# Optimization experiments

Hardware: AMD Instinct MI355X
Metric: run time of the kernel (lower is better)

## Reference

```python
import jax, jax.numpy as jnp
import numpy as np

B, S, H, E = 2, 2048, 16, 64
INV_SCALE = 8.0  # sqrt(head_dim); forward divides scores by this


def setup_inputs() -> dict:
    key = jax.random.key(0)
    ks = jax.random.split(key, 10)
    return {
        "query": jax.random.normal(ks[0], (B, S, H, E), dtype=jnp.float32),
        "key": jax.random.normal(ks[1], (B, S, H, E), dtype=jnp.float32),
        "value": jax.random.normal(ks[2], (B, S, H, E), dtype=jnp.float32),
        "attn_mask": jax.random.randint(ks[3], (B, S), 0, 2, dtype=jnp.int32),
        "Wq": jax.random.normal(ks[4], (E, E), dtype=jnp.float32) / np.sqrt(E),
        "bq": jax.random.normal(ks[5], (E,), dtype=jnp.float32) * 0.02,
        "Wk": jax.random.normal(ks[6], (E, E), dtype=jnp.float32) / np.sqrt(E),
        "bk": jax.random.normal(ks[7], (E,), dtype=jnp.float32) * 0.02,
        "Wv": jax.random.normal(ks[8], (E, E), dtype=jnp.float32) / np.sqrt(E),
        "bv": jax.random.normal(ks[9], (E,), dtype=jnp.float32) * 0.02,
    }


def reference(query, key, value, attn_mask, Wq, bq, Wk, bk, Wv, bv):
    # Linear projections over the last (embed) dim; torch Linear: x @ W.T + b
    q = jnp.einsum('bshe,fe->bhsf', query, Wq) + bq  # [B,H,S,E] (permute 0,2,1,3 fused)
    k = jnp.einsum('bshe,fe->bhsf', key, Wk) + bk
    v = jnp.einsum('bshe,fe->bhsf', value, Wv) + bv
    scores = jnp.einsum('bhqe,bhke->bhqk', q, k) / INV_SCALE  # [B,H,S,S]
    # mask: positions where attn_mask == 0 get -inf, broadcast over (1,1,k_len)
    masked = attn_mask[:, None, None, :] == 0  # [B,1,1,S]
    scores = jnp.where(masked, -jnp.inf, scores)
    attn = jax.nn.softmax(scores, axis=-1)
    out = jnp.einsum('bhqk,bhke->bqhe', attn, v)  # permute back to [B,S,H,E]
    return out
```

## Files before the change

kernel.cpp:

```cpp
#include <hip/hip_runtime.h>


#define BATCH 2
#define SEQ   2048
#define NH    16
#define DE    64
#define LDOF  68
#define NKT   (SEQ / 64)
#define LOG2E 1.44269504088896340736f
#define CSHIFT 16.0f

using bf16x8   = __attribute__((ext_vector_type(8))) __bf16;
using bf16x4   = __attribute__((ext_vector_type(4))) __bf16;
using bf16x2   = __attribute__((ext_vector_type(2))) __bf16;
using floatx2  = __attribute__((ext_vector_type(2))) float;
using floatx4  = __attribute__((ext_vector_type(4))) float;
using floatx16 = __attribute__((ext_vector_type(16))) float;
using ushortx4 = __attribute__((ext_vector_type(4))) unsigned short;
using ushortx8 = __attribute__((ext_vector_type(8))) unsigned short;
using uintx4   = __attribute__((ext_vector_type(4))) unsigned int;
using intx4    = __attribute__((ext_vector_type(4))) int;

__device__ __forceinline__ ushortx4 cvt4(floatx4 f) {
    bf16x4 h = __builtin_convertvector(f, bf16x4);
    return __builtin_bit_cast(ushortx4, h);
}

__device__ __forceinline__ unsigned int pkbf16(float a, float b) {
    floatx2 f = {a, b};
    return __builtin_bit_cast(unsigned int, __builtin_convertvector(f, bf16x2));
}

__device__ __forceinline__ void pl32swap(unsigned int& x, unsigned int& y) {
    __asm__ volatile("v_permlane32_swap_b32 %0, %1" : "+v"(x), "+v"(y));
}

__global__ __launch_bounds__(256) void proj_kernel(
    const float* __restrict__ xq, const float* __restrict__ xk, const float* __restrict__ xv,
    const float* __restrict__ Wq, const float* __restrict__ bq,
    const float* __restrict__ Wk, const float* __restrict__ bk,
    const float* __restrict__ Wv, const float* __restrict__ bv,
    unsigned short* __restrict__ qb, unsigned short* __restrict__ kb,
    unsigned short* __restrict__ vtb)
{
    __shared__ __align__(16) unsigned short Wb[64 * 72];
    __shared__ __align__(16) unsigned short Xb[8 * 1160];
    __shared__ __align__(16) unsigned short Ob[12288];
    __shared__ float blds[64];

    const int t  = threadIdx.x;
    const int bi = blockIdx.x;
    const int hh = bi & 1;
    const int st = (bi >> 1) & 127;
    const int b  = (bi >> 8) & 1;
    const int p  = bi >> 9;
    const int h0 = hh * 8;
    const int lane = t & 63, w = t >> 6, quad = lane >> 4, l16 = lane & 15;

    const float* x    = (p == 0) ? xq : (p == 1) ? xk : xv;
    const float* W    = (p == 0) ? Wq : (p == 1) ? Wk : Wv;
    const float* bias = (p == 0) ? bq : (p == 1) ? bk : bv;

    #pragma unroll
    for (int i = 0; i < 8; ++i) {
        int idx = i * 256 + t;
        int s = idx >> 7, rem = idx & 127, h = rem >> 4, e4 = (rem & 15) * 4;
        floatx4 xv4 = *(const floatx4*)(x + ((size_t)(b * SEQ + st * 16 + s) * NH + h0 + h) * DE + e4);
        *(ushortx4*)&Xb[h * 1160 + s * 72 + e4] = cvt4(xv4);
    }
    #pragma unroll
    for (int i = 0; i < 4; ++i) {
        int idx = i * 256 + t;
        int row = idx >> 4, c4 = (idx & 15) * 4;
        floatx4 wv4 = *(const floatx4*)(W + row * 64 + c4);
        *(ushortx4*)&Wb[row * 72 + c4] = cvt4(wv4);
    }
    if (t < 64) blds[t] = bias[t];
    __syncthreads();

    if (p < 2) {
        bf16x8 a0 = *(const bf16x8*)&Wb[(w * 16 + l16) * 72 + quad * 8];
        bf16x8 a1 = *(const bf16x8*)&Wb[(w * 16 + l16) * 72 + 32 + quad * 8];
        floatx4 bf4 = *(const floatx4*)&blds[w * 16 + quad * 4];
        const float scale = (p == 0) ? 0.125f * LOG2E : 1.0f;
        #pragma unroll
        for (int h = 0; h < 8; ++h) {
            bf16x8 b0 = *(const bf16x8*)&Xb[h * 1160 + l16 * 72 + quad * 8];
            bf16x8 b1 = *(const bf16x8*)&Xb[h * 1160 + l16 * 72 + 32 + quad * 8];
            floatx4 c = {0.f, 0.f, 0.f, 0.f};
            c = __builtin_amdgcn_mfma_f32_16x16x32_bf16(a0, b0, c, 0, 0, 0);
            c = __builtin_amdgcn_mfma_f32_16x16x32_bf16(a1, b1, c, 0, 0, 0);
            floatx4 v;
            v[0] = (c[0] + bf4[0]) * scale; v[1] = (c[1] + bf4[1]) * scale;
            v[2] = (c[2] + bf4[2]) * scale; v[3] = (c[3] + bf4[3]) * scale;
            *(ushortx4*)&Ob[h * 1160 + l16 * 72 + w * 16 + quad * 4] = cvt4(v);
        }
    } else {
        bf16x8 b0 = *(const bf16x8*)&Wb[(w * 16 + l16) * 72 + quad * 8];
        bf16x8 b1 = *(const bf16x8*)&Wb[(w * 16 + l16) * 72 + 32 + quad * 8];
        const float bw = blds[w * 16 + l16];
        #pragma unroll
        for (int h = 0; h < 8; ++h) {
            bf16x8 a0 = *(const bf16x8*)&Xb[h * 1160 + l16 * 72 + quad * 8];
            bf16x8 a1 = *(const bf16x8*)&Xb[h * 1160 + l16 * 72 + 32 + quad * 8];
            floatx4 c = {0.f, 0.f, 0.f, 0.f};
            c = __builtin_amdgcn_mfma_f32_16x16x32_bf16(a0, b0, c, 0, 0, 0);
            c = __builtin_amdgcn_mfma_f32_16x16x32_bf16(a1, b1, c, 0, 0, 0);
            floatx4 v;
            v[0] = c[0] + bw; v[1] = c[1] + bw; v[2] = c[2] + bw; v[3] = c[3] + bw;
            *(ushortx4*)&Ob[h * 1536 + (w * 16 + l16) * 24 + quad * 4] = cvt4(v);
        }
    }
    __syncthreads();

    if (p < 2) {
        unsigned short* dst = (p == 0) ? qb : kb;
        const int rb  = st >> 1;
        const int sl0 = (st & 1) * 16;
        #pragma unroll
        for (int i = 0; i < 4; ++i) {
            int idx = i * 256 + t;
            int j = idx & 7, s = (idx >> 3) & 15, h = idx >> 7;
            ushortx8 v = *(const ushortx8*)&Ob[h * 1160 + s * 72 + j * 8];
            size_t off = ((size_t)((b * 16 + h0 + h) * 64) + rb) * 2048 + j * 256 + (sl0 + s) * 8;
            *(ushortx8*)(dst + off) = v;
        }
    } else {
        const int kt  = st >> 2;
        const int cb  = (st & 3) * 2;
        #pragma unroll
        for (int i = 0; i < 4; ++i) {
            int idx = i * 256 + t;
            int cl = idx & 1, e = (idx >> 1) & 63, h = idx >> 7;
            ushortx8 v = *(const ushortx8*)&Ob[h * 1536 + e * 24 + cl * 8];
            size_t off = (((size_t)(b * 16 + h0 + h) * 32 + kt) * 8 + cb + cl) * 512 + e * 8;
            *(ushortx8*)(vtb + off) = v;
        }
    }
}

__global__ __launch_bounds__(512, 4) void attn_kernel(
    const unsigned short* __restrict__ qb, const unsigned short* __restrict__ kb,
    const unsigned short* __restrict__ vtb, const int* __restrict__ mask,
    float* __restrict__ out)
{
    __shared__ __align__(16) char smem[36864 + 8192];
    float* Ol = (float*)smem;
    float* Ll = (float*)(smem + 34816);
    float* Ml = (float*)(smem + 36864);

    const int wg  = blockIdx.x;
    const int bh  = ((wg >> 3) >> 4) * 8 + (wg & 7);
    const int qt  = (wg >> 3) & 15;
    const int b   = bh >> 4, h = bh & 15;
    const int q0  = qt * 128;
    const int t   = threadIdx.x;
    const int lane = t & 63, w = t >> 6;
    const int hi = lane >> 5, l31 = lane & 31;
    const int qw = w & 3, kblk = w >> 2;

    {
        intx4 mv = *(const intx4*)(mask + b * SEQ + t * 4);
        Ml[t * 4 + 0] = mv[0] ? -CSHIFT : -1e30f;
        Ml[t * 4 + 1] = mv[1] ? -CSHIFT : -1e30f;
        Ml[t * 4 + 2] = mv[2] ? -CSHIFT : -1e30f;
        Ml[t * 4 + 3] = mv[3] ? -CSHIFT : -1e30f;
    }

    const unsigned short* qp = qb + ((size_t)(bh * 64 + qt * 4 + qw)) * 2048 + hi * 256 + l31 * 8;
    bf16x8 qf[4];
    #pragma unroll
    for (int ks = 0; ks < 4; ++ks)
        qf[ks] = *(const bf16x8*)(qp + ks * 512);

    const unsigned short* kp = kb + ((size_t)(bh * 64 + kblk)) * 2048 + hi * 256 + l31 * 8;
    const unsigned short* vp = vtb + (size_t)bh * 131072 + (kblk * 4 + hi) * 512 + l31 * 8;
    const float* Mb = Ml + kblk * 32 + hi * 4;

    __syncthreads();

    floatx16 o0, o1;
    #pragma unroll
    for (int i = 0; i < 16; ++i) { o0[i] = 0.f; o1[i] = 0.f; }
    float lp = 0.f;

    for (int kt = 0; kt < NKT; ++kt) {
        const unsigned short* kq = kp + kt * 4096;
        bf16x8 kf0 = *(const bf16x8*)(kq);
        bf16x8 kf1 = *(const bf16x8*)(kq + 512);
        bf16x8 kf2 = *(const bf16x8*)(kq + 1024);
        bf16x8 kf3 = *(const bf16x8*)(kq + 1536);

        const float* Mc = Mb + kt * 64;
        floatx16 sc;
        #pragma unroll
        for (int g = 0; g < 4; ++g) {
            floatx4 mb = *(const floatx4*)(Mc + g * 8);
            sc[4 * g + 0] = mb[0]; sc[4 * g + 1] = mb[1];
            sc[4 * g + 2] = mb[2]; sc[4 * g + 3] = mb[3];
        }
        sc = __builtin_amdgcn_mfma_f32_32x32x16_bf16(kf0, qf[0], sc, 0, 0, 0);
        sc = __builtin_amdgcn_mfma_f32_32x32x16_bf16(kf1, qf[1], sc, 0, 0, 0);
        sc = __builtin_amdgcn_mfma_f32_32x32x16_bf16(kf2, qf[2], sc, 0, 0, 0);
        sc = __builtin_amdgcn_mfma_f32_32x32x16_bf16(kf3, qf[3], sc, 0, 0, 0);

        const unsigned short* vq = vp + kt * 4096;
        bf16x8 vf00 = *(const bf16x8*)(vq);
        bf16x8 vf01 = *(const bf16x8*)(vq + 256);
        bf16x8 vf10 = *(const bf16x8*)(vq + 1024);
        bf16x8 vf11 = *(const bf16x8*)(vq + 1280);

        #pragma unroll
        for (int r = 0; r < 16; ++r)
            sc[r] = __builtin_amdgcn_exp2f(sc[r]);
        {
            float a0 = sc[0] + sc[1],   a1 = sc[2] + sc[3];
            float a2 = sc[4] + sc[5],   a3 = sc[6] + sc[7];
            float a4 = sc[8] + sc[9],   a5 = sc[10] + sc[11];
            float a6 = sc[12] + sc[13], a7 = sc[14] + sc[15];
            lp += ((a0 + a1) + (a2 + a3)) + ((a4 + a5) + (a6 + a7));
        }

        unsigned int wd0 = pkbf16(sc[0], sc[1]),   wd1 = pkbf16(sc[2], sc[3]);
        unsigned int wd2 = pkbf16(sc[4], sc[5]),   wd3 = pkbf16(sc[6], sc[7]);
        unsigned int wd4 = pkbf16(sc[8], sc[9]),   wd5 = pkbf16(sc[10], sc[11]);
        unsigned int wd6 = pkbf16(sc[12], sc[13]), wd7 = pkbf16(sc[14], sc[15]);
        pl32swap(wd0, wd2); pl32swap(wd1, wd3);
        pl32swap(wd4, wd6); pl32swap(wd5, wd7);
        uintx4 f0v = {wd0, wd1, wd2, wd3};
        uintx4 f1v = {wd4, wd5, wd6, wd7};
        bf16x8 pf0 = __builtin_bit_cast(bf16x8, f0v);
        bf16x8 pf1 = __builtin_bit_cast(bf16x8, f1v);

        o0 = __builtin_amdgcn_mfma_f32_32x32x16_bf16(vf00, pf0, o0, 0, 0, 0);
        o1 = __builtin_amdgcn_mfma_f32_32x32x16_bf16(vf01, pf0, o1, 0, 0, 0);
        o0 = __builtin_amdgcn_mfma_f32_32x32x16_bf16(vf10, pf1, o0, 0, 0, 0);
        o1 = __builtin_amdgcn_mfma_f32_32x32x16_bf16(vf11, pf1, o1, 0, 0, 0);
    }

    const int qrow = qw * 32 + l31;
    Ll[qrow * 4 + kblk * 2 + hi] = lp;
    if (kblk == 1) {
        #pragma unroll
        for (int g = 0; g < 4; ++g) {
            floatx4 t0 = {o0[4*g+0], o0[4*g+1], o0[4*g+2], o0[4*g+3]};
            *(floatx4*)&Ol[qrow * LDOF + g * 8 + hi * 4] = t0;
            floatx4 t1 = {o1[4*g+0], o1[4*g+1], o1[4*g+2], o1[4*g+3]};
            *(floatx4*)&Ol[qrow * LDOF + 32 + g * 8 + hi * 4] = t1;
        }
    }
    __syncthreads();
    if (kblk == 0) {
        floatx4 lv = *(const floatx4*)&Ll[qrow * 4];
        float invl = __builtin_amdgcn_rcpf(lv[0] + lv[1] + lv[2] + lv[3]);
        #pragma unroll
        for (int g = 0; g < 4; ++g) {
            floatx4 t0 = *(floatx4*)&Ol[qrow * LDOF + g * 8 + hi * 4];
            t0[0] = (t0[0] + o0[4*g+0]) * invl; t0[1] = (t0[1] + o0[4*g+1]) * invl;
            t0[2] = (t0[2] + o0[4*g+2]) * invl; t0[3] = (t0[3] + o0[4*g+3]) * invl;
            *(floatx4*)&Ol[qrow * LDOF + g * 8 + hi * 4] = t0;
            floatx4 t1 = *(floatx4*)&Ol[qrow * LDOF + 32 + g * 8 + hi * 4];
            t1[0] = (t1[0] + o1[4*g+0]) * invl; t1[1] = (t1[1] + o1[4*g+1]) * invl;
            t1[2] = (t1[2] + o1[4*g+2]) * invl; t1[3] = (t1[3] + o1[4*g+3]) * invl;
            *(floatx4*)&Ol[qrow * LDOF + 32 + g * 8 + hi * 4] = t1;
        }
    }
    __syncthreads();
    {
        const int quad = lane >> 4, l16 = lane & 15;
        #pragma unroll
        for (int pass = 0; pass < 4; ++pass) {
            int rl  = w * 16 + pass * 4 + quad;
            int col = l16 * 4;
            floatx4 tv = *(const floatx4*)&Ol[rl * LDOF + col];
            *(floatx4*)(out + (((size_t)b * SEQ + q0 + rl) * NH + h) * DE + col) = tv;
        }
    }
}

extern "C" void kernel_launch(void* const* d_in, const int* in_sizes, int n_in,
                              void* d_out, int out_size, void* d_ws, size_t ws_size,
                              hipStream_t stream) {
    const float* query = (const float*)d_in[0];
    const float* key   = (const float*)d_in[1];
    const float* value = (const float*)d_in[2];
    const int*   mask  = (const int*)d_in[3];
    const float* Wq = (const float*)d_in[4];
    const float* bq = (const float*)d_in[5];
    const float* Wk = (const float*)d_in[6];
    const float* bk = (const float*)d_in[7];
    const float* Wv = (const float*)d_in[8];
    const float* bv = (const float*)d_in[9];

    const size_t tensor_elems = (size_t)BATCH * NH * SEQ * DE;
    unsigned short* qb  = (unsigned short*)d_ws;
    unsigned short* kb  = qb + tensor_elems;
    unsigned short* vtb = kb + tensor_elems;

    proj_kernel<<<dim3(3 * BATCH * 128 * 2), 256, 0, stream>>>(
        query, key, value, Wq, bq, Wk, bk, Wv, bv, qb, kb, vtb);
    attn_kernel<<<dim3(512), 512, 0, stream>>>(
        qb, kb, vtb, mask, (float*)d_out);
}
```

Baseline: 152.0 us.

## Split attention waves into two q-rows by four key-split groups with LDS-staged Q

Reorganises the 8 waves of each attention block so that each wave handles two 32-row query tiles (64 rows) against one quarter of the key tiles, instead of one query tile against half the keys. Each K and V fragment loaded from global memory is now reused for two query tiles, which halves K/V global traffic per block. Q is staged into LDS with global_load_lds and read from there, and s_setprio brackets the MFMA groups. The trade-offs are a four-way partial-output reduction in LDS with extra barriers, more accumulator registers (four 16-float accumulators), and LDS reads of Q on every iteration.

```diff
diff --git a/kernel.cpp b/kernel.cpp
--- a/kernel.cpp
+++ b/kernel.cpp
@@ -33,6 +33,12 @@
 
 __device__ __forceinline__ void pl32swap(unsigned int& x, unsigned int& y) {
     __asm__ volatile("v_permlane32_swap_b32 %0, %1" : "+v"(x), "+v"(y));
+}
+
+__device__ __forceinline__ void glds16(const unsigned short* g, unsigned short* l) {
+    __builtin_amdgcn_global_load_lds(
+        (const __attribute__((address_space(1))) unsigned int*)g,
+        (__attribute__((address_space(3))) unsigned int*)l, 16, 0, 0);
 }
 
 __global__ __launch_bounds__(256) void proj_kernel(
@@ -144,10 +150,11 @@
     const unsigned short* __restrict__ vtb, const int* __restrict__ mask,
     float* __restrict__ out)
 {
-    __shared__ __align__(16) char smem[36864 + 8192];
+    __shared__ __align__(16) char smem[38912];
+    unsigned short* Qlds = (unsigned short*)smem;
+    float* Ml = (float*)(smem + 16384);
     float* Ol = (float*)smem;
     float* Ll = (float*)(smem + 34816);
-    float* Ml = (float*)(smem + 36864);
 
     const int wg  = blockIdx.x;
     const int bh  = ((wg >> 3) >> 4) * 8 + (wg & 7);
@@ -157,8 +164,12 @@
     const int t   = threadIdx.x;
     const int lane = t & 63, w = t >> 6;
     const int hi = lane >> 5, l31 = lane & 31;
-    const int qw = w & 3, kblk = w >> 2;
-
+    const int qw = w & 1, kblk = (w >> 1) & 1, par = w >> 2;
+    const int rid = par * 2 + kblk;
+
+    const unsigned short* qsrc = qb + ((size_t)(bh * 64 + qt * 4)) * 2048;
+    glds16(qsrc + w * 512 + lane * 8,        Qlds + w * 512);
+    glds16(qsrc + 4096 + w * 512 + lane * 8, Qlds + 4096 + w * 512);
     {
         intx4 mv = *(const intx4*)(mask + b * SEQ + t * 4);
         Ml[t * 4 + 0] = mv[0] ? -CSHIFT : -1e30f;
@@ -166,103 +177,197 @@
         Ml[t * 4 + 2] = mv[2] ? -CSHIFT : -1e30f;
         Ml[t * 4 + 3] = mv[3] ? -CSHIFT : -1e30f;
     }
-
-    const unsigned short* qp = qb + ((size_t)(bh * 64 + qt * 4 + qw)) * 2048 + hi * 256 + l31 * 8;
-    bf16x8 qf[4];
+    __syncthreads();
+
+    const unsigned short* kp = kb + ((size_t)(bh * 64 + kblk)) * 2048
+                               + (size_t)par * 4096 + hi * 256 + l31 * 8;
+    const unsigned short* vp = vtb + (size_t)bh * 131072 + (size_t)par * 4096
+                               + (kblk * 4 + hi) * 512 + l31 * 8;
+    const float* Mlb = Ml + par * 64 + kblk * 32 + hi * 4;
+    const unsigned short* qba = Qlds + (qw * 2) * 2048 + hi * 256 + l31 * 8;
+
+    floatx16 oa0, oa1, ob0, ob1;
     #pragma unroll
-    for (int ks = 0; ks < 4; ++ks)
-        qf[ks] = *(const bf16x8*)(qp + ks * 512);
-
-    const unsigned short* kp = kb + ((size_t)(bh * 64 + kblk)) * 2048 + hi * 256 + l31 * 8;
-    const unsigned short* vp = vtb + (size_t)bh * 131072 + (kblk * 4 + hi) * 512 + l31 * 8;
-    const float* Mb = Ml + kblk * 32 + hi * 4;
-
-    __syncthreads();
-
-    floatx16 o0, o1;
-    #pragma unroll
-    for (int i = 0; i < 16; ++i) { o0[i] = 0.f; o1[i] = 0.f; }
-    float lp = 0.f;
-
-    for (int kt = 0; kt < NKT; ++kt) {
-        const unsigned short* kq = kp + kt * 4096;
+    for (int i = 0; i < 16; ++i) { oa0[i] = 0.f; oa1[i] = 0.f; ob0[i] = 0.f; ob1[i] = 0.f; }
+    float lpa = 0.f, lpb = 0.f;
+
+    for (int it = 0; it < NKT / 2; ++it) {
+        const unsigned short* kq = kp + (size_t)it * 8192;
         bf16x8 kf0 = *(const bf16x8*)(kq);
         bf16x8 kf1 = *(const bf16x8*)(kq + 512);
         bf16x8 kf2 = *(const bf16x8*)(kq + 1024);
         bf16x8 kf3 = *(const bf16x8*)(kq + 1536);
-
-        const float* Mc = Mb + kt * 64;
-        floatx16 sc;
-        #pragma unroll
-        for (int g = 0; g < 4; ++g) {
-            floatx4 mb = *(const floatx4*)(Mc + g * 8);
-            sc[4 * g + 0] = mb[0]; sc[4 * g + 1] = mb[1];
-            sc[4 * g + 2] = mb[2]; sc[4 * g + 3] = mb[3];
-        }
-        sc = __builtin_amdgcn_mfma_f32_32x32x16_bf16(kf0, qf[0], sc, 0, 0, 0);
-        sc = __builtin_amdgcn_mfma_f32_32x32x16_bf16(kf1, qf[1], sc, 0, 0, 0);
-        sc = __builtin_amdgcn_mfma_f32_32x32x16_bf16(kf2, qf[2], sc, 0, 0, 0);
-        sc = __builtin_amdgcn_mfma_f32_32x32x16_bf16(kf3, qf[3], sc, 0, 0, 0);
-
-        const unsigned short* vq = vp + kt * 4096;
+        const float* Mc = Mlb + it * 128;
+        floatx4 m0 = *(const floatx4*)(Mc);
+        floatx4 m1 = *(const floatx4*)(Mc + 8);
+        floatx4 m2 = *(const floatx4*)(Mc + 16);
+        floatx4 m3 = *(const floatx4*)(Mc + 24);
+
+        floatx16 sa;
+        #pragma unroll
+        for (int j = 0; j < 4; ++j) {
+            sa[j] = m0[j]; sa[4 + j] = m1[j]; sa[8 + j] = m2[j]; sa[12 + j] = m3[j];
+        }
+        __builtin_amdgcn_s_setprio(1);
+        sa = __builtin_amdgcn_mfma_f32_32x32x16_bf16(kf0, *(const bf16x8*)(qba), sa, 0, 0, 0);
+        sa = __builtin_amdgcn_mfma_f32_32x32x16_bf16(kf1, *(const bf16x8*)(qba + 512), sa, 0, 0, 0);
+        sa = __builtin_amdgcn_mfma_f32_32x32x16_bf16(kf2, *(const bf16x8*)(qba + 1024), sa, 0, 0, 0);
+        sa = __builtin_amdgcn_mfma_f32_32x32x16_bf16(kf3, *(const bf16x8*)(qba + 1536), sa, 0, 0, 0);
+        __builtin_amdgcn_s_setprio(0);
+        #pragma unroll
+        for (int r = 0; r < 16; ++r) sa[r] = __builtin_amdgcn_exp2f(sa[r]);
+        {
+            float a0 = sa[0] + sa[1],   a1 = sa[2] + sa[3];
+            float a2 = sa[4] + sa[5],   a3 = sa[6] + sa[7];
+            float a4 = sa[8] + sa[9],   a5 = sa[10] + sa[11];
+            float a6 = sa[12] + sa[13], a7 = sa[14] + sa[15];
+            lpa += ((a0 + a1) + (a2 + a3)) + ((a4 + a5) + (a6 + a7));
+        }
+        unsigned int aw0 = pkbf16(sa[0], sa[1]),   aw1 = pkbf16(sa[2], sa[3]);
+        unsigned int aw2 = pkbf16(sa[4], sa[5]),   aw3 = pkbf16(sa[6], sa[7]);
+        unsigned int aw4 = pkbf16(sa[8], sa[9]),   aw5 = pkbf16(sa[10], sa[11]);
+        unsigned int aw6 = pkbf16(sa[12], sa[13]), aw7 = pkbf16(sa[14], sa[15]);
+        pl32swap(aw0, aw2); pl32swap(aw1, aw3);
+        pl32swap(aw4, aw6); pl32swap(aw5, aw7);
+        uintx4 fa0 = {aw0, aw1, aw2, aw3};
+        uintx4 fa1 = {aw4, aw5, aw6, aw7};
+        bf16x8 pf0a = __builtin_bit_cast(bf16x8, fa0);
+        bf16x8 pf1a = __builtin_bit_cast(bf16x8, fa1);
+
+        floatx16 sb;
+        #pragma unroll
+        for (int j = 0; j < 4; ++j) {
+            sb[j] = m0[j]; sb[4 + j] = m1[j]; sb[8 + j] = m2[j]; sb[12 + j] = m3[j];
+        }
+        __builtin_amdgcn_s_setprio(1);
+        sb = __builtin_amdgcn_mfma_f32_32x32x16_bf16(kf0, *(const bf16x8*)(qba + 2048), sb, 0, 0, 0);
+        sb = __builtin_amdgcn_mfma_f32_32x32x16_bf16(kf1, *(const bf16x8*)(qba + 2560), sb, 0, 0, 0);
+        sb = __builtin_amdgcn_mfma_f32_32x32x16_bf16(kf2, *(const bf16x8*)(qba + 3072), sb, 0, 0, 0);
+        sb = __builtin_amdgcn_mfma_f32_32x32x16_bf16(kf3, *(const bf16x8*)(qba + 3584), sb, 0, 0, 0);
+        __builtin_amdgcn_s_setprio(0);
+
+        const unsigned short* vq = vp + (size_t)it * 8192;
         bf16x8 vf00 = *(const bf16x8*)(vq);
         bf16x8 vf01 = *(const bf16x8*)(vq + 256);
         bf16x8 vf10 = *(const bf16x8*)(vq + 1024);
         bf16x8 vf11 = *(const bf16x8*)(vq + 1280);
 
         #pragma unroll
-        for (int r = 0; r < 16; ++r)
-            sc[r] = __builtin_amdgcn_exp2f(sc[r]);
+        for (int r = 0; r < 16; ++r) sb[r] = __builtin_amdgcn_exp2f(sb[r]);
         {
-            float a0 = sc[0] + sc[1],   a1 = sc[2] + sc[3];
-            float a2 = sc[4] + sc[5],   a3 = sc[6] + sc[7];
-            float a4 = sc[8] + sc[9],   a5 = sc[10] + sc[11];
-            float a6 = sc[12] + sc[13], a7 = sc[14] + sc[15];
-            lp += ((a0 + a1) + (a2 + a3)) + ((a4 + a5) + (a6 + a7));
-        }
-
-        unsigned int wd0 = pkbf16(sc[0], sc[1]),   wd1 = pkbf16(sc[2], sc[3]);
-        unsigned int wd2 = pkbf16(sc[4], sc[5]),   wd3 = pkbf16(sc[6], sc[7]);
-        unsigned int wd4 = pkbf16(sc[8], sc[9]),   wd5 = pkbf16(sc[10], sc[11]);
-        unsigned int wd6 = pkbf16(sc[12], sc[13]), wd7 = pkbf16(sc[14], sc[15]);
-        pl32swap(wd0, wd2); pl32swap(wd1, wd3);
-        pl32swap(wd4, wd6); pl32swap(wd5, wd7);
-        uintx4 f0v = {wd0, wd1, wd2, wd3};
-        uintx4 f1v = {wd4, wd5, wd6, wd7};
-        bf16x8 pf0 = __builtin_bit_cast(bf16x8, f0v);
-        bf16x8 pf1 = __builtin_bit_cast(bf16x8, f1v);
-
-        o0 = __builtin_amdgcn_mfma_f32_32x32x16_bf16(vf00, pf0, o0, 0, 0, 0);
-        o1 = __builtin_amdgcn_mfma_f32_32x32x16_bf16(vf01, pf0, o1, 0, 0, 0);
-        o0 = __builtin_amdgcn_mfma_f32_32x32x16_bf16(vf10, pf1, o0, 0, 0, 0);
-        o1 = __builtin_amdgcn_mfma_f32_32x32x16_bf16(vf11, pf1, o1, 0, 0, 0);
-    }
-
-    const int qrow = qw * 32 + l31;
-    Ll[qrow * 4 + kblk * 2 + hi] = lp;
-    if (kblk == 1) {
+            float b0 = sb[0] + sb[1],   b1 = sb[2] + sb[3];
+            float b2 = sb[4] + sb[5],   b3 = sb[6] + sb[7];
+            float b4 = sb[8] + sb[9],   b5 = sb[10] + sb[11];
+            float b6 = sb[12] + sb[13], b7 = sb[14] + sb[15];
+            lpb += ((b0 + b1) + (b2 + b3)) + ((b4 + b5) + (b6 + b7));
+        }
+        unsigned int bw0 = pkbf16(sb[0], sb[1]),   bw1 = pkbf16(sb[2], sb[3]);
+        unsigned int bw2 = pkbf16(sb[4], sb[5]),   bw3 = pkbf16(sb[6], sb[7]);
+        unsigned int bw4 = pkbf16(sb[8], sb[9]),   bw5 = pkbf16(sb[10], sb[11]);
+        unsigned int bw6 = pkbf16(sb[12], sb[13]), bw7 = pkbf16(sb[14], sb[15]);
+        pl32swap(bw0, bw2); pl32swap(bw1, bw3);
+        pl32swap(bw4, bw6); pl32swap(bw5, bw7);
+        uintx4 fb0 = {bw0, bw1, bw2, bw3};
+        uintx4 fb1 = {bw4, bw5, bw6, bw7};
+        bf16x8 pf0b = __builtin_bit_cast(bf16x8, fb0);
+        bf16x8 pf1b = __builtin_bit_cast(bf16x8, fb1);
+
+        __builtin_amdgcn_s_setprio(1);
+        oa0 = __builtin_amdgcn_mfma_f32_32x32x16_bf16(vf00, pf0a, oa0, 0, 0, 0);
+        oa1 = __builtin_amdgcn_mfma_f32_32x32x16_bf16(vf01, pf0a, oa1, 0, 0, 0);
+        oa0 = __builtin_amdgcn_mfma_f32_32x32x16_bf16(vf10, pf1a, oa0, 0, 0, 0);
+        oa1 = __builtin_amdgcn_mfma_f32_32x32x16_bf16(vf11, pf1a, oa1, 0, 0, 0);
+        ob0 = __builtin_amdgcn_mfma_f32_32x32x16_bf16(vf00, pf0b, ob0, 0, 0, 0);
+        ob1 = __builtin_amdgcn_mfma_f32_32x32x16_bf16(vf01, pf0b, ob1, 0, 0, 0);
+        ob0 = __builtin_amdgcn_mfma_f32_32x32x16_bf16(vf10, pf1b, ob0, 0, 0, 0);
+        ob1 = __builtin_amdgcn_mfma_f32_32x32x16_bf16(vf11, pf1b, ob1, 0, 0, 0);
+        __builtin_amdgcn_s_setprio(0);
+    }
+
+    const int qa  = qw * 64 + l31;
+    const int qrb = qa + 32;
+    Ll[qa * 8 + rid * 2 + hi]  = lpa;
+    Ll[qrb * 8 + rid * 2 + hi] = lpb;
+    __syncthreads();
+    if (rid == 3) {
         #pragma unroll
         for (int g = 0; g < 4; ++g) {
-            floatx4 t0 = {o0[4*g+0], o0[4*g+1], o0[4*g+2], o0[4*g+3]};
-            *(floatx4*)&Ol[qrow * LDOF + g * 8 + hi * 4] = t0;
-            floatx4 t1 = {o1[4*g+0], o1[4*g+1], o1[4*g+2], o1[4*g+3]};
-            *(floatx4*)&Ol[qrow * LDOF + 32 + g * 8 + hi * 4] = t1;
-        }
-    }
-    __syncthreads();
-    if (kblk == 0) {
-        floatx4 lv = *(const floatx4*)&Ll[qrow * 4];
-        float invl = __builtin_amdgcn_rcpf(lv[0] + lv[1] + lv[2] + lv[3]);
+            floatx4 t0 = {oa0[4*g+0], oa0[4*g+1], oa0[4*g+2], oa0[4*g+3]};
+            *(floatx4*)&Ol[qa * LDOF + g * 8 + hi * 4] = t0;
+            floatx4 t1 = {oa1[4*g+0], oa1[4*g+1], oa1[4*g+2], oa1[4*g+3]};
+            *(floatx4*)&Ol[qa * LDOF + 32 + g * 8 + hi * 4] = t1;
+            floatx4 t2 = {ob0[4*g+0], ob0[4*g+1], ob0[4*g+2], ob0[4*g+3]};
+            *(floatx4*)&Ol[qrb * LDOF + g * 8 + hi * 4] = t2;
+            floatx4 t3 = {ob1[4*g+0], ob1[4*g+1], ob1[4*g+2], ob1[4*g+3]};
+            *(floatx4*)&Ol[qrb * LDOF + 32 + g * 8 + hi * 4] = t3;
+        }
+    }
+    __syncthreads();
+    if (rid == 2 || rid == 1) {
+        if (rid == 2) {
+            #pragma unroll
+            for (int g = 0; g < 4; ++g) {
+                floatx4 t0 = *(floatx4*)&Ol[qa * LDOF + g * 8 + hi * 4];
+                t0[0] += oa0[4*g+0]; t0[1] += oa0[4*g+1]; t0[2] += oa0[4*g+2]; t0[3] += oa0[4*g+3];
+                *(floatx4*)&Ol[qa * LDOF + g * 8 + hi * 4] = t0;
+                floatx4 t1 = *(floatx4*)&Ol[qa * LDOF + 32 + g * 8 + hi * 4];
+                t1[0] += oa1[4*g+0]; t1[1] += oa1[4*g+1]; t1[2] += oa1[4*g+2]; t1[3] += oa1[4*g+3];
+                *(floatx4*)&Ol[qa * LDOF + 32 + g * 8 + hi * 4] = t1;
+                floatx4 t2 = *(floatx4*)&Ol[qrb * LDOF + g * 8 + hi * 4];
+                t2[0] += ob0[4*g+0]; t2[1] += ob0[4*g+1]; t2[2] += ob0[4*g+2]; t2[3] += ob0[4*g+3];
+                *(floatx4*)&Ol[qrb * LDOF + g * 8 + hi * 4] = t2;
+                floatx4 t3 = *(floatx4*)&Ol[qrb * LDOF + 32 + g * 8 + hi * 4];
+                t3[0] += ob1[4*g+0]; t3[1] += ob1[4*g+1]; t3[2] += ob1[4*g+2]; t3[3] += ob1[4*g+3];
+                *(floatx4*)&Ol[qrb * LDOF + 32 + g * 8 + hi * 4] = t3;
+            }
+        }
+    }
+    __syncthreads();
+    if (rid == 1) {
         #pragma unroll
         for (int g = 0; g < 4; ++g) {
-            floatx4 t0 = *(floatx4*)&Ol[qrow * LDOF + g * 8 + hi * 4];
-            t0[0] = (t0[0] + o0[4*g+0]) * invl; t0[1] = (t0[1] + o0[4*g+1]) * invl;
-            t0[2] = (t0[2] + o0[4*g+2]) * invl; t0[3] = (t0[3] + o0[4*g+3]) * invl;
-            *(floatx4*)&Ol[qrow * LDOF + g * 8 + hi * 4] = t0;
-            floatx4 t1 = *(floatx4*)&Ol[qrow * LDOF + 32 + g * 8 + hi * 4];
-            t1[0] = (t1[0] + o1[4*g+0]) * invl; t1[1] = (t1[1] + o1[4*g+1]) * invl;
-            t1[2] = (t1[2] + o1[4*g+2]) * invl; t1[3] = (t1[3] + o1[4*g+3]) * invl;
-            *(floatx4*)&Ol[qrow * LDOF + 32 + g * 8 + hi * 4] = t1;
+            floatx4 t0 = *(floatx4*)&Ol[qa * LDOF + g * 8 + hi * 4];
+            t0[0] += oa0[4*g+0]; t0[1] += oa0[4*g+1]; t0[2] += oa0[4*g+2]; t0[3] += oa0[4*g+3];
+            *(floatx4*)&Ol[qa * LDOF + g * 8 + hi * 4] = t0;
+            floatx4 t1 = *(floatx4*)&Ol[qa * LDOF + 32 + g * 8 + hi * 4];
+            t1[0] += oa1[4*g+0]; t1[1] += oa1[4*g+1]; t1[2] += oa1[4*g+2]; t1[3] += oa1[4*g+3];
+            *(floatx4*)&Ol[qa * LDOF + 32 + g * 8 + hi * 4] = t1;
+            floatx4 t2 = *(floatx4*)&Ol[qrb * LDOF + g * 8 + hi * 4];
+            t2[0] += ob0[4*g+0]; t2[1] += ob0[4*g+1]; t2[2] += ob0[4*g+2]; t2[3] += ob0[4*g+3];
+            *(floatx4*)&Ol[qrb * LDOF + g * 8 + hi * 4] = t2;
+            floatx4 t3 = *(floatx4*)&Ol[qrb * LDOF + 32 + g * 8 + hi * 4];
+            t3[0] += ob1[4*g+0]; t3[1] += ob1[4*g+1]; t3[2] += ob1[4*g+2]; t3[3] += ob1[4*g+3];
+            *(floatx4*)&Ol[qrb * LDOF + 32 + g * 8 + hi * 4] = t3;
+        }
+    }
+    __syncthreads();
+    if (rid == 0) {
+        floatx4 la0 = *(const floatx4*)&Ll[qa * 8];
+        floatx4 la1 = *(const floatx4*)&Ll[qa * 8 + 4];
+        float invla = __builtin_amdgcn_rcpf(la0[0] + la0[1] + la0[2] + la0[3]
+                                          + la1[0] + la1[1] + la1[2] + la1[3]);
+        floatx4 lb0 = *(const floatx4*)&Ll[qrb * 8];
+        floatx4 lb1 = *(const floatx4*)&Ll[qrb * 8 + 4];
+        float invlb = __builtin_amdgcn_rcpf(lb0[0] + lb0[1] + lb0[2] + lb0[3]
+                                          + lb1[0] + lb1[1] + lb1[2] + lb1[3]);
+        #pragma unroll
+        for (int g = 0; g < 4; ++g) {
+            floatx4 t0 = *(floatx4*)&Ol[qa * LDOF + g * 8 + hi * 4];
+            t0[0] = (t0[0] + oa0[4*g+0]) * invla; t0[1] = (t0[1] + oa0[4*g+1]) * invla;
+            t0[2] = (t0[2] + oa0[4*g+2]) * invla; t0[3] = (t0[3] + oa0[4*g+3]) * invla;
+            *(floatx4*)&Ol[qa * LDOF + g * 8 + hi * 4] = t0;
+            floatx4 t1 = *(floatx4*)&Ol[qa * LDOF + 32 + g * 8 + hi * 4];
+            t1[0] = (t1[0] + oa1[4*g+0]) * invla; t1[1] = (t1[1] + oa1[4*g+1]) * invla;
+            t1[2] = (t1[2] + oa1[4*g+2]) * invla; t1[3] = (t1[3] + oa1[4*g+3]) * invla;
+            *(floatx4*)&Ol[qa * LDOF + 32 + g * 8 + hi * 4] = t1;
+            floatx4 t2 = *(floatx4*)&Ol[qrb * LDOF + g * 8 + hi * 4];
+            t2[0] = (t2[0] + ob0[4*g+0]) * invlb; t2[1] = (t2[1] + ob0[4*g+1]) * invlb;
+            t2[2] = (t2[2] + ob0[4*g+2]) * invlb; t2[3] = (t2[3] + ob0[4*g+3]) * invlb;
+            *(floatx4*)&Ol[qrb * LDOF + g * 8 + hi * 4] = t2;
+            floatx4 t3 = *(floatx4*)&Ol[qrb * LDOF + 32 + g * 8 + hi * 4];
+            t3[0] = (t3[0] + ob1[4*g+0]) * invlb; t3[1] = (t3[1] + ob1[4*g+1]) * invlb;
+            t3[2] = (t3[2] + ob1[4*g+2]) * invlb; t3[3] = (t3[3] + ob1[4*g+3]) * invlb;
+            *(floatx4*)&Ol[qrb * LDOF + 32 + g * 8 + hi * 4] = t3;
         }
     }
     __syncthreads();
```

After: 259.9 us. +71.0%, slower.
